# Kernel optimization log

Measured on AMD Instinct MI355X. Metric: run time of the kernel, lower is better.

The kernel has to match this reference:

```python
import jax, jax.numpy as jnp
import numpy as np

EMBED_DIM = 1024
BOTTLENECK = 48          # adapter_hidden_dim (adapter_rank=0)
ADAPTER_WIDTH = 1        # multivector channels
MV_DIM = 16              # Cl(1,3) multivector dimension
N_GRADES = 5             # grades of sizes 1,4,6,4,1
LN_EPS = 1e-5

# grade projection mask [5,16]: grade0=idx0, grade1=1:5, grade2=5:11, grade3=11:15, grade4=15
_gm = np.zeros((N_GRADES, MV_DIM), dtype=np.float32)
_gm[0, 0] = 1.0
_gm[1, 1:5] = 1.0
_gm[2, 5:11] = 1.0
_gm[3, 11:15] = 1.0
_gm[4, 15] = 1.0
GRADE_MASK = jnp.asarray(_gm)


def setup_inputs() -> dict:
    key = jax.random.key(0)
    ks = jax.random.split(key, 8)
    B, N, D, R, W = 128, 256, EMBED_DIM, BOTTLENECK, ADAPTER_WIDTH
    x = jax.random.normal(ks[0], (B, N, D), dtype=jnp.float32)
    gamma = jnp.ones((D,), dtype=jnp.float32)
    beta = jnp.zeros((D,), dtype=jnp.float32)
    w_down = jax.random.normal(ks[1], (R, D), dtype=jnp.float32) / np.sqrt(D)
    w_to_mv = jax.random.normal(ks[2], (W * MV_DIM, R), dtype=jnp.float32) / np.sqrt(R)
    w_equi = jax.random.normal(ks[3], (W, W, N_GRADES), dtype=jnp.float32)
    b_equi = jnp.zeros((W,), dtype=jnp.float32)
    w_from_mv = jax.random.normal(ks[4], (R, W * MV_DIM), dtype=jnp.float32) / np.sqrt(W * MV_DIM)
    w_up = jax.random.normal(ks[5], (D, R), dtype=jnp.float32) / np.sqrt(R)
    scale = jnp.float32(0.001)
    return {"x": x, "gamma": gamma, "beta": beta, "w_down": w_down,
            "w_to_mv": w_to_mv, "w_equi": w_equi, "b_equi": b_equi,
            "w_from_mv": w_from_mv, "w_up": w_up, "scale": scale}


def reference(x, gamma, beta, w_down, w_to_mv, w_equi, b_equi, w_from_mv, w_up, scale):
    B, N, D = x.shape
    # LayerNorm
    mu = jnp.mean(x, axis=-1, keepdims=True)
    var = jnp.mean(jnp.square(x - mu), axis=-1, keepdims=True)
    h = (x - mu) * jax.lax.rsqrt(var + LN_EPS) * gamma + beta
    # down + GELU (exact, matching torch F.gelu default)
    h = jax.nn.gelu(jnp.einsum('bnd,rd->bnr', h, w_down), approximate=False)
    # to multivectors [B,N,C,16]
    mv = jnp.einsum('bnr,mr->bnm', h, w_to_mv).reshape(B, N, -1, MV_DIM)
    # EquiLinear: per-grade channel mixing + scalar bias
    mv = jnp.einsum('oik,kj,bnij->bnoj', w_equi, GRADE_MASK, mv)
    mv = mv.at[..., 0].add(b_equi)
    # from multivectors + GELU
    h = jax.nn.gelu(jnp.einsum('bnm,rm->bnr', mv.reshape(B, N, -1), w_from_mv),
                    approximate=False)
    # up (dropout p=0 is identity) and scaled residual
    h = jnp.einsum('bnr,dr->bnd', h, w_up)
    return x + scale * h
```

## Files before the change

### kernel.cpp

```cpp
#include <hip/hip_runtime.h>
#include <hip/hip_bf16.h>


typedef __attribute__((ext_vector_type(8))) short short8;
typedef __attribute__((ext_vector_type(4))) short short4b;
typedef __attribute__((ext_vector_type(4))) float float4a;

#define NTOK 32768
#define D 1024
#define NBLK 1024

__device__ __forceinline__ short f2bf(float x) {
    unsigned u = __float_as_uint(x);
    unsigned r = u + 0x7FFFu + ((u >> 16) & 1u);
    return (short)(r >> 16);
}
__device__ __forceinline__ float bf2f(short s) {
    return __uint_as_float(((unsigned)(unsigned short)s) << 16);
}
__device__ __forceinline__ float gelu_exact(float v) {
    return 0.5f * v * (1.0f + erff(v * 0.70710678118654752f));
}

__device__ __forceinline__ void bar_lds() {
    asm volatile("s_waitcnt lgkmcnt(0)" ::: "memory");
    __builtin_amdgcn_s_barrier();
    asm volatile("" ::: "memory");
}

__global__ void prep_weights(const float* __restrict__ wdn_f, const float* __restrict__ wup_f,
                             const float* __restrict__ gamma, const float* __restrict__ beta,
                             short* __restrict__ wdn_b, short* __restrict__ wup_b,
                             float* __restrict__ c12) {
    int blk = blockIdx.x;
    int tid = threadIdx.x;
    if (blk < 192) {
        int o = blk * 256 + tid;
        int j = o & 7, lane = (o >> 3) & 63, kt = (o >> 9) & 31, cb = o >> 14;
        int r = cb * 16 + (lane & 15);
        int d = kt * 32 + (lane >> 4) * 8 + j;
        wdn_b[o] = f2bf(wdn_f[r * 1024 + d] * gamma[d]);
    } else if (blk < 448) {
        int o2 = (blk - 192) * 256 + tid;
        int j = o2 & 7, lane = (o2 >> 3) & 63, kt = (o2 >> 9) & 1, cb = o2 >> 10;
        int dcol = cb * 16 + (lane & 15);
        int r = kt * 32 + (lane >> 4) * 8 + j;
        wup_b[o2] = (r < 48) ? f2bf(wup_f[dcol * 48 + r]) : (short)0;
    } else {
        int r = blk - 448;
        float a = 0.f, b = 0.f;
#pragma unroll
        for (int i = 0; i < 4; ++i) {
            int d = tid + 256 * i;
            float wv = wdn_f[r * 1024 + d];
            a = fmaf(wv, gamma[d], a);
            b = fmaf(wv, beta[d], b);
        }
#pragma unroll
        for (int off = 32; off; off >>= 1) {
            a += __shfl_xor(a, off);
            b += __shfl_xor(b, off);
        }
        __shared__ float red[8];
        int lane = tid & 63, w = tid >> 6;
        if (lane == 0) { red[w] = a; red[4 + w] = b; }
        __syncthreads();
        if (tid == 0) {
            c12[r]      = red[0] + red[1] + red[2] + red[3];
            c12[48 + r] = red[4] + red[5] + red[6] + red[7];
        }
    }
}

__launch_bounds__(256, 4)
__global__ void adapter_main(const float* __restrict__ x, const float* __restrict__ w_to_mv,
                             const float* __restrict__ w_equi, const float* __restrict__ b_equi,
                             const float* __restrict__ w_from_mv, const float* __restrict__ scale_p,
                             const short* __restrict__ wdn_b, const short* __restrict__ wup_b,
                             const float* __restrict__ c12, float* __restrict__ out) {
    __shared__ __align__(16) short xsh[16][1032];
    __shared__ __align__(16) float scratch[1568];
    short* zbuf = (short*)scratch;

    const int tid  = threadIdx.x;
    const int lane = tid & 63;
    const int w    = tid >> 6;
    const int q    = lane >> 4;
    const int m    = lane & 15;
    const long tokbase = (long)blockIdx.x * 32;
    const float scale = scale_p[0];

    const float4* xr = (const float4*)(x + tokbase * D);
    float4 v[16];
#pragma unroll
    for (int t = 0; t < 4; ++t)
#pragma unroll
        for (int i = 0; i < 4; ++i)
            v[t * 4 + i] = xr[(w * 4 + t) * 256 + lane + 64 * i];

#pragma unroll
    for (int c = 0; c < 2; ++c) {
        const long token0 = tokbase + c * 16;

#pragma unroll
        for (int t = 0; t < 4; ++t) {
            int tok = w * 4 + t;
            float s1 = 0.f, s2 = 0.f;
#pragma unroll
            for (int i = 0; i < 4; ++i) {
                float4 vv = v[t * 4 + i];
                s1 += vv.x + vv.y + vv.z + vv.w;
                s2 += vv.x * vv.x + vv.y * vv.y + vv.z * vv.z + vv.w * vv.w;
            }
#pragma unroll
            for (int off = 32; off; off >>= 1) {
                s1 += __shfl_xor(s1, off);
                s2 += __shfl_xor(s2, off);
            }
            float mu  = s1 * (1.0f / 1024.0f);
            float var = fmaf(-mu, mu, s2 * (1.0f / 1024.0f));
            float rs  = rsqrtf(var + 1e-5f);
#pragma unroll
            for (int i = 0; i < 4; ++i) {
                int d0 = 4 * lane + 256 * i;
                float4 vv = v[t * 4 + i];
                short4b xs = {f2bf(vv.x), f2bf(vv.y), f2bf(vv.z), f2bf(vv.w)};
                *(short4b*)&xsh[tok][d0] = xs;
            }
            if (lane == 0) {
                scratch[1536 + tok] = rs;
                scratch[1552 + tok] = -mu * rs;
            }
        }

        float4 vn[16];
        if (c == 0) {
            const float4* xr2 = (const float4*)(x + (tokbase + 16) * D);
#pragma unroll
            for (int t = 0; t < 4; ++t)
#pragma unroll
                for (int i = 0; i < 4; ++i)
                    vn[t * 4 + i] = xr2[(w * 4 + t) * 256 + lane + 64 * i];
        }
        bar_lds();

#pragma unroll
        for (int rep = 0; rep < 2; ++rep) {
            int jid = w + rep * 4;
            if (jid < 6) {
                int cb = jid % 3, kh = jid / 3;
                float4a acc = {0.f, 0.f, 0.f, 0.f};
                const short* bptr = wdn_b + ((cb * 32 + kh * 16) * 64 + lane) * 8;
                const short* aptr = &xsh[m][kh * 512 + q * 8];
#pragma unroll
                for (int kt = 0; kt < 16; ++kt) {
                    short8 a = *(const short8*)(aptr + kt * 32);
                    short8 b = *(const short8*)(bptr + kt * 512);
                    acc = __builtin_amdgcn_mfma_f32_16x16x32_bf16(a, b, acc, 0, 0, 0);
                }
#pragma unroll
                for (int i = 0; i < 4; ++i)
                    scratch[kh * 768 + (q * 4 + i) * 48 + cb * 16 + m] = acc[i];
            }
        }
        bar_lds();

#pragma unroll
        for (int k = 0; k < 3; ++k) {
            int it = tid + k * 256;
            int tt = it / 48, r = it - tt * 48;
            float s = scratch[tt * 48 + r] + scratch[768 + tt * 48 + r];
            float y = fmaf(scratch[1536 + tt], s, fmaf(scratch[1552 + tt], c12[r], c12[48 + r]));
            scratch[tt * 48 + r] = gelu_exact(y);
        }
        bar_lds();
        {
            int tt = tid >> 4, j = tid & 15;
            float acc = 0.f;
#pragma unroll 8
            for (int r = 0; r < 48; ++r) acc = fmaf(w_to_mv[j * 48 + r], scratch[tt * 48 + r], acc);
            int g = (j == 0) ? 0 : (j < 5) ? 1 : (j < 11) ? 2 : (j < 15) ? 3 : 4;
            acc *= w_equi[g];
            if (j == 0) acc += b_equi[0];
            scratch[768 + tt * 16 + j] = acc;
        }
        bar_lds();
#pragma unroll
        for (int k = 0; k < 3; ++k) {
            int it = tid + k * 256;
            int tt = it / 48, r = it - tt * 48;
            float acc = 0.f;
#pragma unroll
            for (int j = 0; j < 16; ++j) acc = fmaf(w_from_mv[r * 16 + j], scratch[768 + tt * 16 + j], acc);
            float z = gelu_exact(acc);
            int kt = r >> 5, qq = (r >> 3) & 3, jj = r & 7;
            zbuf[kt * 512 + (qq * 16 + tt) * 8 + jj] = f2bf(z);
        }
        zbuf[768 + tid] = 0;
        bar_lds();

        short8 a0 = *(const short8*)&zbuf[lane * 8];
        short8 a1 = *(const short8*)&zbuf[512 + lane * 8];
        long rowbase = (token0 + q * 4) * D;
#pragma unroll 4
        for (int cc = 0; cc < 16; ++cc) {
            int cb = w * 16 + cc;
            short8 b0 = *(const short8*)(wup_b + (cb * 2 + 0) * 512 + lane * 8);
            short8 b1 = *(const short8*)(wup_b + (cb * 2 + 1) * 512 + lane * 8);
            float4a acc = {0.f, 0.f, 0.f, 0.f};
            acc = __builtin_amdgcn_mfma_f32_16x16x32_bf16(a0, b0, acc, 0, 0, 0);
            acc = __builtin_amdgcn_mfma_f32_16x16x32_bf16(a1, b1, acc, 0, 0, 0);
            int d = cb * 16 + m;
#pragma unroll
            for (int i = 0; i < 4; ++i) {
                int tok = q * 4 + i;
                float xv = bf2f(xsh[tok][d]);
                out[rowbase + (long)i * D + d] = fmaf(scale, acc[i], xv);
            }
        }

        if (c == 0) {
            bar_lds();
#pragma unroll
            for (int i2 = 0; i2 < 16; ++i2) v[i2] = vn[i2];
        }
    }
}

extern "C" void kernel_launch(void* const* d_in, const int* in_sizes, int n_in,
                              void* d_out, int out_size, void* d_ws, size_t ws_size,
                              hipStream_t stream) {
    const float* x         = (const float*)d_in[0];
    const float* gamma     = (const float*)d_in[1];
    const float* beta      = (const float*)d_in[2];
    const float* w_down    = (const float*)d_in[3];
    const float* w_to_mv   = (const float*)d_in[4];
    const float* w_equi    = (const float*)d_in[5];
    const float* b_equi    = (const float*)d_in[6];
    const float* w_from_mv = (const float*)d_in[7];
    const float* w_up      = (const float*)d_in[8];
    const float* scale_p   = (const float*)d_in[9];

    short* wdn_b = (short*)d_ws;
    short* wup_b = wdn_b + 49152;
    float* c12   = (float*)(wup_b + 65536);

    prep_weights<<<496, 256, 0, stream>>>(w_down, w_up, gamma, beta, wdn_b, wup_b, c12);
    adapter_main<<<NBLK, 256, 0, stream>>>(
        x, w_to_mv, w_equi, b_equi, w_from_mv, scale_p,
        wdn_b, wup_b, c12, (float*)d_out);
}
```

Measured before the change: 283.4 us.

## Shrink adapter blocks to 8 tokens and drop two-chunk prefetch pipeline

```diff
diff --git a/kernel.cpp b/kernel.cpp
--- a/kernel.cpp
+++ b/kernel.cpp
@@ -8,7 +8,8 @@
 
 #define NTOK 32768
 #define D 1024
-#define NBLK 1024
+#define TOK 8
+#define NBLK (NTOK / TOK)
 
 __device__ __forceinline__ short f2bf(float x) {
     unsigned u = __float_as_uint(x);
@@ -72,14 +73,14 @@
     }
 }
 
-__launch_bounds__(256, 4)
+__launch_bounds__(256, 8)
 __global__ void adapter_main(const float* __restrict__ x, const float* __restrict__ w_to_mv,
                              const float* __restrict__ w_equi, const float* __restrict__ b_equi,
                              const float* __restrict__ w_from_mv, const float* __restrict__ scale_p,
                              const short* __restrict__ wdn_b, const short* __restrict__ wup_b,
                              const float* __restrict__ c12, float* __restrict__ out) {
-    __shared__ __align__(16) short xsh[16][1032];
-    __shared__ __align__(16) float scratch[1568];
+    __shared__ __align__(16) short xsh[TOK][1032];
+    __shared__ __align__(16) float scratch[912];
     short* zbuf = (short*)scratch;
 
     const int tid  = threadIdx.x;
@@ -87,24 +88,20 @@
     const int w    = tid >> 6;
     const int q    = lane >> 4;
     const int m    = lane & 15;
-    const long tokbase = (long)blockIdx.x * 32;
-    const float scale = scale_p[0];
-
-    const float4* xr = (const float4*)(x + tokbase * D);
-    float4 v[16];
-#pragma unroll
-    for (int t = 0; t < 4; ++t)
-#pragma unroll
-        for (int i = 0; i < 4; ++i)
-            v[t * 4 + i] = xr[(w * 4 + t) * 256 + lane + 64 * i];
-
-#pragma unroll
-    for (int c = 0; c < 2; ++c) {
-        const long token0 = tokbase + c * 16;
-
-#pragma unroll
-        for (int t = 0; t < 4; ++t) {
-            int tok = w * 4 + t;
+    const long token0 = (long)blockIdx.x * TOK;
+
+    {
+        const float4* xr = (const float4*)(x + token0 * D);
+        float4 v[8];
+#pragma unroll
+        for (int t = 0; t < 2; ++t)
+#pragma unroll
+            for (int i = 0; i < 4; ++i)
+                v[t * 4 + i] = xr[(w * 2 + t) * 256 + lane + 64 * i];
+
+#pragma unroll
+        for (int t = 0; t < 2; ++t) {
+            int tok = w * 2 + t;
             float s1 = 0.f, s2 = 0.f;
 #pragma unroll
             for (int i = 0; i < 4; ++i) {
@@ -128,101 +125,95 @@
                 *(short4b*)&xsh[tok][d0] = xs;
             }
             if (lane == 0) {
-                scratch[1536 + tok] = rs;
-                scratch[1552 + tok] = -mu * rs;
-            }
-        }
-
-        float4 vn[16];
-        if (c == 0) {
-            const float4* xr2 = (const float4*)(x + (tokbase + 16) * D);
-#pragma unroll
-            for (int t = 0; t < 4; ++t)
+                scratch[896 + tok] = rs;
+                scratch[904 + tok] = -mu * rs;
+            }
+        }
+    }
+    bar_lds();
+
+#pragma unroll
+    for (int rep = 0; rep < 2; ++rep) {
+        int jid = w + rep * 4;
+        if (jid < 6) {
+            int cb = jid % 3, kh = jid / 3;
+            float4a acc = {0.f, 0.f, 0.f, 0.f};
+            const short* bptr = wdn_b + ((cb * 32 + kh * 16) * 64 + lane) * 8;
+            const short* aptr = &xsh[m & 7][kh * 512 + q * 8];
+#pragma unroll
+            for (int kt = 0; kt < 16; ++kt) {
+                short8 a = *(const short8*)(aptr + kt * 32);
+                short8 b = *(const short8*)(bptr + kt * 512);
+                acc = __builtin_amdgcn_mfma_f32_16x16x32_bf16(a, b, acc, 0, 0, 0);
+            }
+            if (q < 2) {
 #pragma unroll
                 for (int i = 0; i < 4; ++i)
-                    vn[t * 4 + i] = xr2[(w * 4 + t) * 256 + lane + 64 * i];
-        }
-        bar_lds();
-
-#pragma unroll
-        for (int rep = 0; rep < 2; ++rep) {
-            int jid = w + rep * 4;
-            if (jid < 6) {
-                int cb = jid % 3, kh = jid / 3;
-                float4a acc = {0.f, 0.f, 0.f, 0.f};
-                const short* bptr = wdn_b + ((cb * 32 + kh * 16) * 64 + lane) * 8;
-                const short* aptr = &xsh[m][kh * 512 + q * 8];
-#pragma unroll
-                for (int kt = 0; kt < 16; ++kt) {
-                    short8 a = *(const short8*)(aptr + kt * 32);
-                    short8 b = *(const short8*)(bptr + kt * 512);
-                    acc = __builtin_amdgcn_mfma_f32_16x16x32_bf16(a, b, acc, 0, 0, 0);
-                }
-#pragma unroll
-                for (int i = 0; i < 4; ++i)
-                    scratch[kh * 768 + (q * 4 + i) * 48 + cb * 16 + m] = acc[i];
-            }
-        }
-        bar_lds();
-
-#pragma unroll
-        for (int k = 0; k < 3; ++k) {
-            int it = tid + k * 256;
+                    scratch[kh * 384 + (q * 4 + i) * 48 + cb * 16 + m] = acc[i];
+            }
+        }
+    }
+    bar_lds();
+
+#pragma unroll
+    for (int k = 0; k < 2; ++k) {
+        int it = tid + k * 256;
+        if (it < 384) {
             int tt = it / 48, r = it - tt * 48;
-            float s = scratch[tt * 48 + r] + scratch[768 + tt * 48 + r];
-            float y = fmaf(scratch[1536 + tt], s, fmaf(scratch[1552 + tt], c12[r], c12[48 + r]));
-            scratch[tt * 48 + r] = gelu_exact(y);
-        }
-        bar_lds();
-        {
-            int tt = tid >> 4, j = tid & 15;
-            float acc = 0.f;
+            float s = scratch[it] + scratch[384 + it];
+            float y = fmaf(scratch[896 + tt], s, fmaf(scratch[904 + tt], c12[r], c12[48 + r]));
+            scratch[it] = gelu_exact(y);
+        }
+    }
+    bar_lds();
+    if (tid < 128) {
+        int tt = tid >> 4, j = tid & 15;
+        float acc = 0.f;
 #pragma unroll 8
-            for (int r = 0; r < 48; ++r) acc = fmaf(w_to_mv[j * 48 + r], scratch[tt * 48 + r], acc);
-            int g = (j == 0) ? 0 : (j < 5) ? 1 : (j < 11) ? 2 : (j < 15) ? 3 : 4;
-            acc *= w_equi[g];
-            if (j == 0) acc += b_equi[0];
-            scratch[768 + tt * 16 + j] = acc;
-        }
-        bar_lds();
-#pragma unroll
-        for (int k = 0; k < 3; ++k) {
-            int it = tid + k * 256;
+        for (int r = 0; r < 48; ++r) acc = fmaf(w_to_mv[j * 48 + r], scratch[tt * 48 + r], acc);
+        int g = (j == 0) ? 0 : (j < 5) ? 1 : (j < 11) ? 2 : (j < 15) ? 3 : 4;
+        acc *= w_equi[g];
+        if (j == 0) acc += b_equi[0];
+        scratch[768 + tt * 16 + j] = acc;
+    }
+    bar_lds();
+#pragma unroll
+    for (int k = 0; k < 2; ++k) {
+        int it = tid + k * 256;
+        if (it < 384) {
             int tt = it / 48, r = it - tt * 48;
             float acc = 0.f;
 #pragma unroll
-            for (int j = 0; j < 16; ++j) acc = fmaf(w_from_mv[r * 16 + j], scratch[768 + tt * 16 + j], acc);
+            for (int j = 0; j < 16; ++j)
+                acc = fmaf(w_from_mv[r * 16 + j], scratch[768 + tt * 16 + j], acc);
             float z = gelu_exact(acc);
             int kt = r >> 5, qq = (r >> 3) & 3, jj = r & 7;
             zbuf[kt * 512 + (qq * 16 + tt) * 8 + jj] = f2bf(z);
         }
-        zbuf[768 + tid] = 0;
-        bar_lds();
-
-        short8 a0 = *(const short8*)&zbuf[lane * 8];
-        short8 a1 = *(const short8*)&zbuf[512 + lane * 8];
-        long rowbase = (token0 + q * 4) * D;
+    }
+    zbuf[768 + tid] = 0;
+    bar_lds();
+
+    const float scale = scale_p[0];
+    short8 a0 = *(const short8*)&zbuf[lane * 8];
+    short8 a1 = *(const short8*)&zbuf[512 + lane * 8];
+    long rowbase = (token0 + q * 4) * D;
 #pragma unroll 4
-        for (int cc = 0; cc < 16; ++cc) {
-            int cb = w * 16 + cc;
-            short8 b0 = *(const short8*)(wup_b + (cb * 2 + 0) * 512 + lane * 8);
-            short8 b1 = *(const short8*)(wup_b + (cb * 2 + 1) * 512 + lane * 8);
-            float4a acc = {0.f, 0.f, 0.f, 0.f};
-            acc = __builtin_amdgcn_mfma_f32_16x16x32_bf16(a0, b0, acc, 0, 0, 0);
-            acc = __builtin_amdgcn_mfma_f32_16x16x32_bf16(a1, b1, acc, 0, 0, 0);
-            int d = cb * 16 + m;
+    for (int cc = 0; cc < 16; ++cc) {
+        int cb = w * 16 + cc;
+        short8 b0 = *(const short8*)(wup_b + (cb * 2 + 0) * 512 + lane * 8);
+        short8 b1 = *(const short8*)(wup_b + (cb * 2 + 1) * 512 + lane * 8);
+        float4a acc = {0.f, 0.f, 0.f, 0.f};
+        acc = __builtin_amdgcn_mfma_f32_16x16x32_bf16(a0, b0, acc, 0, 0, 0);
+        acc = __builtin_amdgcn_mfma_f32_16x16x32_bf16(a1, b1, acc, 0, 0, 0);
+        int d = cb * 16 + m;
+        if (q < 2) {
 #pragma unroll
             for (int i = 0; i < 4; ++i) {
                 int tok = q * 4 + i;
                 float xv = bf2f(xsh[tok][d]);
                 out[rowbase + (long)i * D + d] = fmaf(scale, acc[i], xv);
             }
-        }
-
-        if (c == 0) {
-            bar_lds();
-#pragma unroll
-            for (int i2 = 0; i2 < 16; ++i2) v[i2] = vn[i2];
         }
     }
 }
```

Result: faster. 277.6 us (-2.0%).
